# Performance work log

Measured on AMD Instinct MI355X. Metric: run time of the kernel, lower is better.

Reference implementation:

```python
import jax, jax.numpy as jnp
import numpy as np

Q = 4          # num_quantizers
K = 2048       # codebook_size
D = 256        # dim
B, N = 8, 8192 # batch, tokens (N % Q == 0)


def l2norm(t, eps=1e-12):
    return t / jnp.maximum(jnp.linalg.norm(t, axis=-1, keepdims=True), eps)


def setup_inputs() -> dict:
    key = jax.random.key(0)
    kx, ke = jax.random.split(key)
    x = jax.random.normal(kx, (B, N, D), dtype=jnp.float32)
    embed = jax.random.normal(ke, (Q, K, D), dtype=jnp.float32)
    return {"x": x, "embed": embed}


def reference(x, embed):
    b, n, d = x.shape
    q = embed.shape[0]
    m = n // q  # tokens per quantizer chunk
    # chunk along token axis (dim=1), as torch.chunk(x, Q, dim=1)
    xc = x.reshape(b, q, m, d).transpose(1, 0, 2, 3)  # [Q, B, M, D]

    def one_vq(xq, eq):
        # xq: [B, M, D], eq: [K, D]
        xn = l2norm(xq)
        en = l2norm(eq)
        dist = jnp.einsum('bmd,kd->bmk', xn, en)   # cosine similarity
        ind = jnp.argmax(dist, axis=-1)            # temp=0 gumbel -> argmax
        quant = eq[ind]                            # F.embedding with raw embed
        return quant, ind

    quant_c, ind_c = jax.vmap(one_vq)(xc, embed)   # [Q,B,M,D], [Q,B,M]
    quantized = quant_c.transpose(1, 0, 2, 3).reshape(b, n, d)
    encoding = ind_c.transpose(1, 0, 2).reshape(b, n)
    # eval mode: loss is sum of Q zero tensors of shape [1]
    vq_loss = jnp.zeros((1,), dtype=x.dtype)
    return quantized, encoding, vq_loss
```

## Files before the change

### kernel.cpp

```cpp
#include <hip/hip_runtime.h>
#include <math.h>

#define Bq 8
#define Nq 8192
#define Dq 256
#define Qq 4
#define Kq 2048
#define Mq (Nq / Qq)
#define TT (Bq * Nq)
#define QUANT_ELEMS ((size_t)TT * Dq)

#define CAP1Q 4096
#define THRESH 3e-4f

#define WS_CNT_OFF    0u
#define WS_LIST_OFF   1024u
#define WS_PSC_OFF    66560u
#define WS_PCD_OFF    590848u
#define WS_ENH_OFF    1115136u
#define WS_ENP_OFF    5309440u
#define WS_PART_OFF   13698048u

typedef __attribute__((ext_vector_type(8))) _Float16 f16x8;
typedef __attribute__((ext_vector_type(4))) _Float16 f16x4;
typedef __attribute__((ext_vector_type(4))) float    f32x4;

__device__ __forceinline__ void async_load16(const void* g, void* s) {
    __builtin_amdgcn_global_load_lds(
        (const __attribute__((address_space(1))) void*)g,
        (__attribute__((address_space(3))) void*)s, 16, 0, 0);
}

__device__ __forceinline__ float f32_div(float a, float b) {
    return (float)((double)a / (double)b);
}

__device__ __forceinline__ float np_norm_wave(const float* __restrict__ src, int ln) {
#pragma clang fp contract(off)
    float r = 0.0f;
    if (ln < 16) {
        const float* p = src + (ln >> 3) * 128 + (ln & 7);
        #pragma unroll
        for (int m = 0; m < 16; ++m) { float v = p[m * 8]; r = r + v * v; }
    }
    float t = r + __shfl_xor(r, 1, 64);
    t = t + __shfl_xor(t, 2, 64);
    t = t + __shfl_xor(t, 4, 64);
    float b0 = __shfl(t, 0, 64);
    float b1 = __shfl(t, 8, 64);
    float n2 = b0 + b1;
    return fmaxf((float)sqrt((double)n2), 1e-12f);
}

__global__ __launch_bounds__(256) void prep_kernel(const float* __restrict__ embed,
                                                   char* __restrict__ enh,
                                                   float* __restrict__ enp) {
    int row = blockIdx.x * 4 + (threadIdx.x >> 6);
    int ln  = threadIdx.x & 63;
    const float* src = embed + (size_t)row * Dq;

    float4 v = *(const float4*)(src + ln * 4);
    float s = v.x * v.x + v.y * v.y + v.z * v.z + v.w * v.w;
    #pragma unroll
    for (int m = 1; m < 64; m <<= 1) s += __shfl_xor(s, m, 64);
    float sx = 1.0f / fmaxf(sqrtf(s), 1e-12f);
    int q = row >> 11, k = row & 2047, Tb = k >> 5, c = k & 31;
    int g = ln >> 1, h = ln & 1;
    f16x4 o;
    o[0] = (_Float16)(v.x * sx); o[1] = (_Float16)(v.y * sx);
    o[2] = (_Float16)(v.z * sx); o[3] = (_Float16)(v.w * sx);
    char* dst = enh + ((size_t)(q * 64 + Tb)) * 16384 + c * 512 + ((g ^ c) << 4) + h * 8;
    *(f16x4*)dst = o;

    float nm = np_norm_wave(src, ln);
    float* dstp = enp + (size_t)row * Dq;
    #pragma unroll
    for (int e = 0; e < 4; ++e) dstp[ln * 4 + e] = f32_div(src[ln * 4 + e], nm);
}

__global__ __launch_bounds__(256) void gemm_kernel(const float* __restrict__ x,
                                                   const char* __restrict__ enh,
                                                   float4* __restrict__ part) {
    __shared__ __align__(16) char es[2][16384];

    const int tid = threadIdx.x;
    const int wv  = tid >> 6;
    const int ln  = tid & 63;
    const int qd  = ln >> 4;
    const int l15 = ln & 15;

    const int bid = blockIdx.x;
    const int q   = bid & 3;
    const int h   = (bid >> 2) & 1;
    const int w   = bid >> 3;
    const int t0  = (w >> 4) * Nq + q * Mq + (w & 15) * 128;
    const int t0w = t0 + wv * 32;

    f16x8 ah[2][8];
    #pragma unroll
    for (int mf = 0; mf < 2; ++mf) {
        const float* xr = x + (size_t)(t0w + mf * 16 + l15) * Dq + qd * 8;
        float4 xa[16];
        float s2 = 0.f;
        #pragma unroll
        for (int ch = 0; ch < 8; ++ch) {
            float4 u = *(const float4*)(xr + ch * 32);
            float4 v = *(const float4*)(xr + ch * 32 + 4);
            xa[2 * ch] = u; xa[2 * ch + 1] = v;
            s2 += u.x * u.x + u.y * u.y + u.z * u.z + u.w * u.w;
            s2 += v.x * v.x + v.y * v.y + v.z * v.z + v.w * v.w;
        }
        s2 += __shfl_xor(s2, 16, 64);
        s2 += __shfl_xor(s2, 32, 64);
        float sx = 1.0f / fmaxf(sqrtf(s2), 1e-12f);
        #pragma unroll
        for (int ch = 0; ch < 8; ++ch) {
            float4 u = xa[2 * ch], v = xa[2 * ch + 1];
            f16x8 f;
            f[0] = (_Float16)(u.x * sx); f[1] = (_Float16)(u.y * sx);
            f[2] = (_Float16)(u.z * sx); f[3] = (_Float16)(u.w * sx);
            f[4] = (_Float16)(v.x * sx); f[5] = (_Float16)(v.y * sx);
            f[6] = (_Float16)(v.z * sx); f[7] = (_Float16)(v.w * sx);
            ah[mf][ch] = f;
        }
    }

    float b1[2][4], b2[2][4];
    int   ic[2][4];
    #pragma unroll
    for (int mf = 0; mf < 2; ++mf)
        #pragma unroll
        for (int r = 0; r < 4; ++r) { b1[mf][r] = -2.0f; b2[mf][r] = -2.0f; ic[mf][r] = 0; }

    const char* ebase = enh + ((size_t)(q * 64 + h * 32)) * 16384;

    #pragma unroll
    for (int i = 0; i < 4; ++i) {
        int off = i * 4096 + wv * 1024 + ln * 16;
        async_load16(ebase + off, es[0] + off);
    }
    __syncthreads();

    for (int T = 0; T < 32; ++T) {
        if (T + 1 < 32) {
            const char* src = ebase + (size_t)(T + 1) * 16384;
            #pragma unroll
            for (int i = 0; i < 4; ++i) {
                int off = i * 4096 + wv * 1024 + ln * 16;
                async_load16(src + off, es[(T + 1) & 1] + off);
            }
        }
        const char* esb = es[T & 1];

        #pragma unroll
        for (int s = 0; s < 2; ++s) {
            const int  c  = s * 16 + l15;
            const char* cb = esb + c * 512;
            f16x8 bfr[8];
            #pragma unroll
            for (int ch = 0; ch < 8; ++ch)
                bfr[ch] = *(const f16x8*)(cb + ((((ch << 2) | qd) ^ c) << 4));

            f32x4 a0 = {0.f, 0.f, 0.f, 0.f};
            f32x4 a1 = {0.f, 0.f, 0.f, 0.f};
            #pragma unroll
            for (int ch = 0; ch < 8; ++ch) {
                a0 = __builtin_amdgcn_mfma_f32_16x16x32_f16(ah[0][ch], bfr[ch], a0, 0, 0, 0);
                a1 = __builtin_amdgcn_mfma_f32_16x16x32_f16(ah[1][ch], bfr[ch], a1, 0, 0, 0);
            }
            const int cg = (h << 10) | (T << 5) | (s << 4) | l15;
            #pragma unroll
            for (int r = 0; r < 4; ++r) {
                float s0 = a0[r];
                bool  g0 = s0 > b1[0][r];
                b2[0][r] = __builtin_amdgcn_fmed3f(s0, b1[0][r], b2[0][r]);
                b1[0][r] = fmaxf(b1[0][r], s0);
                ic[0][r] = g0 ? cg : ic[0][r];
                float s1 = a1[r];
                bool  g1 = s1 > b1[1][r];
                b2[1][r] = __builtin_amdgcn_fmed3f(s1, b1[1][r], b2[1][r]);
                b1[1][r] = fmaxf(b1[1][r], s1);
                ic[1][r] = g1 ? cg : ic[1][r];
            }
        }
        __syncthreads();
    }

    float fb1[2][4], fb2[2][4];
    int   fic[2][4];
    #pragma unroll
    for (int mf = 0; mf < 2; ++mf)
        #pragma unroll
        for (int r = 0; r < 4; ++r) {
            float v1 = b1[mf][r], v2 = b2[mf][r]; int vi = ic[mf][r];
            #pragma unroll
            for (int m = 1; m < 16; m <<= 1) {
                float o1 = __shfl_xor(v1, m, 64);
                float o2 = __shfl_xor(v2, m, 64);
                int   oi = __shfl_xor(vi, m, 64);
                if (o1 > v1 || (o1 == v1 && oi < vi)) { v2 = fmaxf(v1, o2); v1 = o1; vi = oi; }
                else v2 = fmaxf(v2, o1);
            }
            fb1[mf][r] = v1; fb2[mf][r] = v2; fic[mf][r] = vi;
        }

    if (l15 == 0) {
        #pragma unroll
        for (int mf = 0; mf < 2; ++mf)
            #pragma unroll
            for (int r = 0; r < 4; ++r) {
                int t = t0w + mf * 16 + qd * 4 + r;
                float4 pv;
                pv.x = fb1[mf][r];
                pv.y = fb2[mf][r];
                pv.z = __int_as_float(fic[mf][r]);
                pv.w = 0.f;
                part[(size_t)h * TT + t] = pv;
            }
    }
}

__global__ __launch_bounds__(256) void merge_kernel(const float* __restrict__ embed,
                                                    const float4* __restrict__ part,
                                                    float* __restrict__ out,
                                                    int* __restrict__ cnt,
                                                    int* __restrict__ list) {
    const int wv = threadIdx.x >> 6, ln = threadIdx.x & 63;
    const int nw = gridDim.x * 4;

    for (int t = blockIdx.x * 4 + wv; t < TT; t += nw) {
        float4 pa = part[t];
        float4 pb = part[TT + t];
        float v1, v2; int vi;
        if (pb.x > pa.x) { v1 = pb.x; vi = __float_as_int(pb.z); v2 = fmaxf(pa.x, pb.y); }
        else             { v1 = pa.x; vi = __float_as_int(pa.z); v2 = fmaxf(pb.x, pa.y); }
        const int q = (t >> 11) & 3;

        if (ln == 0) {
            out[QUANT_ELEMS + (size_t)t] = (float)vi;
            if (v1 - v2 < THRESH) {
                int pos = atomicAdd(&cnt[q], 1);
                if (pos < CAP1Q) list[q * CAP1Q + pos] = t;
            }
        }
        const float* er = embed + ((size_t)(q * Kq + vi)) * Dq;
        float4 v = *(const float4*)(er + ln * 4);
        *(float4*)(out + (size_t)t * Dq + ln * 4) = v;
    }
    if (blockIdx.x == 0 && threadIdx.x == 0) out[QUANT_ELEMS + TT] = 0.0f;
}

__global__ __launch_bounds__(256) void fix_partial(const float* __restrict__ x,
                                                   const float* __restrict__ enp,
                                                   const int* __restrict__ cnt,
                                                   const int* __restrict__ list,
                                                   float* __restrict__ pscore,
                                                   int* __restrict__ pcode) {
#pragma clang fp contract(off)
    __shared__ float xn[16][Dq];
    __shared__ int   stok[16];
    __shared__ float wp_s[4][16];
    __shared__ int   wp_c[4][16];

    const int tid = threadIdx.x;
    const int wv  = tid >> 6;
    const int ln  = tid & 63;

    int cq[4], nbq[4], total = 0;
    #pragma unroll
    for (int q = 0; q < 4; ++q) {
        int c = cnt[q]; if (c > CAP1Q) c = CAP1Q;
        cq[q] = c; nbq[q] = (c + 15) >> 4; total += nbq[q] * 8;
    }

    for (int j = blockIdx.x; j < total; j += gridDim.x) {
        int rem = j, q = 0;
        while (rem >= nbq[q] * 8) { rem -= nbq[q] * 8; ++q; }
        const int batch = rem >> 3, chunk = rem & 7;

        if (tid < 16) {
            int idx = batch * 16 + tid;
            stok[tid] = list[q * CAP1Q + (idx < cq[q] ? idx : batch * 16)];
        }
        __syncthreads();
        for (int r = 0; r < 4; ++r) {
            int i = wv * 4 + r;
            const float* xr = x + (size_t)stok[i] * Dq;
            float nm = np_norm_wave(xr, ln);
            #pragma unroll
            for (int e = 0; e < 4; ++e)
                xn[i][ln * 4 + e] = f32_div(xr[ln * 4 + e], nm);
        }
        __syncthreads();

        const int c = chunk * 256 + tid;
        const float* er = enp + ((size_t)(q * Kq + c)) * Dq;
        float l0[16], l1[16], l2[16], l3[16];
        #pragma unroll
        for (int i = 0; i < 16; ++i) { l0[i] = 0.f; l1[i] = 0.f; l2[i] = 0.f; l3[i] = 0.f; }

        for (int d = 0; d < Dq; d += 4) {
            float4 e = *(const float4*)(er + d);
            #pragma unroll
            for (int i = 0; i < 16; ++i) {
                float4 xv = *(const float4*)&xn[i][d];
                l0[i] = l0[i] + xv.x * e.x;
                l1[i] = l1[i] + xv.y * e.y;
                l2[i] = l2[i] + xv.z * e.z;
                l3[i] = l3[i] + xv.w * e.w;
            }
        }

        #pragma unroll
        for (int i = 0; i < 16; ++i) {
            float s = (l0[i] + l1[i]) + (l2[i] + l3[i]);
            int bc = c;
            #pragma unroll
            for (int m = 1; m < 64; m <<= 1) {
                float os = __shfl_xor(s, m, 64);
                int   oc = __shfl_xor(bc, m, 64);
                if (os > s || (os == s && oc < bc)) { s = os; bc = oc; }
            }
            if (ln == 0) { wp_s[wv][i] = s; wp_c[wv][i] = bc; }
        }
        __syncthreads();
        if (tid < 16) {
            int idx = batch * 16 + tid;
            if (idx < cq[q]) {
                float s = wp_s[0][tid]; int bc = wp_c[0][tid];
                #pragma unroll
                for (int w2 = 1; w2 < 4; ++w2) {
                    float os = wp_s[w2][tid]; int oc = wp_c[w2][tid];
                    if (os > s || (os == s && oc < bc)) { s = os; bc = oc; }
                }
                int p = q * CAP1Q + idx;
                pscore[p * 8 + chunk] = s;
                pcode[p * 8 + chunk]  = bc;
            }
        }
        __syncthreads();
    }
}

__global__ __launch_bounds__(256) void fix_final(const float* __restrict__ embed,
                                                 const int* __restrict__ cnt,
                                                 const int* __restrict__ list,
                                                 const float* __restrict__ pscore,
                                                 const int* __restrict__ pcode,
                                                 float* __restrict__ out) {
    int cq[4], tot = 0;
    #pragma unroll
    for (int q = 0; q < 4; ++q) {
        int c = cnt[q]; if (c > CAP1Q) c = CAP1Q;
        cq[q] = c; tot += c;
    }
    const int wv = threadIdx.x >> 6, ln = threadIdx.x & 63;

    for (int j = blockIdx.x * 4 + wv; j < tot; j += gridDim.x * 4) {
        int rem = j, q = 0;
        while (rem >= cq[q]) { rem -= cq[q]; ++q; }
        int p = q * CAP1Q + rem;
        int t = list[p];
        int bc = 0;
        if (ln == 0) {
            float bs = pscore[p * 8]; bc = pcode[p * 8];
            #pragma unroll
            for (int ch = 1; ch < 8; ++ch) {
                float s = pscore[p * 8 + ch]; int c2 = pcode[p * 8 + ch];
                if (s > bs || (s == bs && c2 < bc)) { bs = s; bc = c2; }
            }
            out[QUANT_ELEMS + (size_t)t] = (float)bc;
        }
        bc = __shfl(bc, 0, 64);
        const float* er = embed + ((size_t)(q * Kq + bc)) * Dq;
        float4 v = *(const float4*)(er + ln * 4);
        *(float4*)(out + (size_t)t * Dq + ln * 4) = v;
    }
}

extern "C" void kernel_launch(void* const* d_in, const int* in_sizes, int n_in,
                              void* d_out, int out_size, void* d_ws, size_t ws_size,
                              hipStream_t stream) {
    const float* x     = (const float*)d_in[0];
    const float* embed = (const float*)d_in[1];
    float* out = (float*)d_out;
    char*  ws  = (char*)d_ws;
    int*    cnt    = (int*)(ws + WS_CNT_OFF);
    int*    list   = (int*)(ws + WS_LIST_OFF);
    float*  pscore = (float*)(ws + WS_PSC_OFF);
    int*    pcode  = (int*)(ws + WS_PCD_OFF);
    char*   enh    = ws + WS_ENH_OFF;
    float*  enp    = (float*)(ws + WS_ENP_OFF);
    float4* part   = (float4*)(ws + WS_PART_OFF);

    hipMemsetAsync(cnt, 0, 16, stream);
    prep_kernel<<<(Qq * Kq) / 4, 256, 0, stream>>>(embed, enh, enp);
    gemm_kernel<<<1024, 256, 0, stream>>>(x, enh, part);
    merge_kernel<<<2048, 256, 0, stream>>>(embed, part, out, cnt, list);
    fix_partial<<<1024, 256, 0, stream>>>(x, enp, cnt, list, pscore, pcode);
    fix_final<<<256, 256, 0, stream>>>(embed, cnt, list, pscore, pcode, out);
}
```

Measured before the change: 290.1 us.

## Use triple-buffered half-size LDS tiles with explicit vmcnt waits in GEMM loop

The codebook tile loop changes from double-buffered 16 KB tiles to a three-stage ring of 8 KB tiles (16 codes each), prefetching two tiles ahead. Each step waits with an explicit s_waitcnt vmcnt and a single barrier instead of two __syncthreads per tile. This is meant to hide global-to-LDS latency better and cut shared memory use per block, which could allow more blocks per CU. In exchange there are twice as many barrier steps, each doing less MFMA work, and the hand-written vmcnt counting relies on the async_load16 instruction count staying fixed.

Measured after the change: 298.1 us. +2.8%, slower.

```diff
diff --git a/kernel.cpp b/kernel.cpp
--- a/kernel.cpp
+++ b/kernel.cpp
@@ -81,7 +81,7 @@
 __global__ __launch_bounds__(256) void gemm_kernel(const float* __restrict__ x,
                                                    const char* __restrict__ enh,
                                                    float4* __restrict__ part) {
-    __shared__ __align__(16) char es[2][16384];
+    __shared__ __align__(16) char es[3][8192];
 
     const int tid = threadIdx.x;
     const int wv  = tid >> 6;
@@ -133,57 +133,60 @@
         for (int r = 0; r < 4; ++r) { b1[mf][r] = -2.0f; b2[mf][r] = -2.0f; ic[mf][r] = 0; }
 
     const char* ebase = enh + ((size_t)(q * 64 + h * 32)) * 16384;
-
-    #pragma unroll
-    for (int i = 0; i < 4; ++i) {
-        int off = i * 4096 + wv * 1024 + ln * 16;
-        async_load16(ebase + off, es[0] + off);
-    }
-    __syncthreads();
-
-    for (int T = 0; T < 32; ++T) {
-        if (T + 1 < 32) {
-            const char* src = ebase + (size_t)(T + 1) * 16384;
-            #pragma unroll
-            for (int i = 0; i < 4; ++i) {
-                int off = i * 4096 + wv * 1024 + ln * 16;
-                async_load16(src + off, es[(T + 1) & 1] + off);
-            }
-        }
-        const char* esb = es[T & 1];
-
-        #pragma unroll
-        for (int s = 0; s < 2; ++s) {
-            const int  c  = s * 16 + l15;
-            const char* cb = esb + c * 512;
-            f16x8 bfr[8];
-            #pragma unroll
-            for (int ch = 0; ch < 8; ++ch)
-                bfr[ch] = *(const f16x8*)(cb + ((((ch << 2) | qd) ^ c) << 4));
-
-            f32x4 a0 = {0.f, 0.f, 0.f, 0.f};
-            f32x4 a1 = {0.f, 0.f, 0.f, 0.f};
-            #pragma unroll
-            for (int ch = 0; ch < 8; ++ch) {
-                a0 = __builtin_amdgcn_mfma_f32_16x16x32_f16(ah[0][ch], bfr[ch], a0, 0, 0, 0);
-                a1 = __builtin_amdgcn_mfma_f32_16x16x32_f16(ah[1][ch], bfr[ch], a1, 0, 0, 0);
-            }
-            const int cg = (h << 10) | (T << 5) | (s << 4) | l15;
-            #pragma unroll
-            for (int r = 0; r < 4; ++r) {
-                float s0 = a0[r];
-                bool  g0 = s0 > b1[0][r];
-                b2[0][r] = __builtin_amdgcn_fmed3f(s0, b1[0][r], b2[0][r]);
-                b1[0][r] = fmaxf(b1[0][r], s0);
-                ic[0][r] = g0 ? cg : ic[0][r];
-                float s1 = a1[r];
-                bool  g1 = s1 > b1[1][r];
-                b2[1][r] = __builtin_amdgcn_fmed3f(s1, b1[1][r], b2[1][r]);
-                b1[1][r] = fmaxf(b1[1][r], s1);
-                ic[1][r] = g1 ? cg : ic[1][r];
-            }
-        }
-        __syncthreads();
+    const int off0 = wv * 1024 + ln * 16;
+
+    #pragma unroll
+    for (int i = 0; i < 2; ++i)
+        async_load16(ebase + i * 4096 + off0, es[0] + i * 4096 + off0);
+    #pragma unroll
+    for (int i = 0; i < 2; ++i)
+        async_load16(ebase + 8192 + i * 4096 + off0, es[1] + i * 4096 + off0);
+
+    int rb = 0;
+    for (int T = 0; T < 64; ++T) {
+        if (T < 63) asm volatile("s_waitcnt vmcnt(2)" ::: "memory");
+        else        asm volatile("s_waitcnt vmcnt(0)" ::: "memory");
+        __builtin_amdgcn_s_barrier();
+        asm volatile("" ::: "memory");
+
+        if (T + 2 < 64) {
+            int wb = rb + 2; if (wb >= 3) wb -= 3;
+            const char* src = ebase + (size_t)(T + 2) * 8192;
+            #pragma unroll
+            for (int i = 0; i < 2; ++i)
+                async_load16(src + i * 4096 + off0, es[wb] + i * 4096 + off0);
+        }
+
+        const char* cb = es[rb] + l15 * 512;
+        const int   c5 = ((T & 1) << 4) | l15;
+        f16x8 bfr[8];
+        #pragma unroll
+        for (int ch = 0; ch < 8; ++ch)
+            bfr[ch] = *(const f16x8*)(cb + ((((ch << 2) | qd) ^ c5) << 4));
+
+        f32x4 a0 = {0.f, 0.f, 0.f, 0.f};
+        f32x4 a1 = {0.f, 0.f, 0.f, 0.f};
+        #pragma unroll
+        for (int ch = 0; ch < 8; ++ch) {
+            a0 = __builtin_amdgcn_mfma_f32_16x16x32_f16(ah[0][ch], bfr[ch], a0, 0, 0, 0);
+            a1 = __builtin_amdgcn_mfma_f32_16x16x32_f16(ah[1][ch], bfr[ch], a1, 0, 0, 0);
+        }
+
+        const int cg = (h << 10) | (T << 4) | l15;
+        #pragma unroll
+        for (int r = 0; r < 4; ++r) {
+            float s0 = a0[r];
+            bool  g0 = s0 > b1[0][r];
+            b2[0][r] = __builtin_amdgcn_fmed3f(s0, b1[0][r], b2[0][r]);
+            b1[0][r] = fmaxf(b1[0][r], s0);
+            ic[0][r] = g0 ? cg : ic[0][r];
+            float s1 = a1[r];
+            bool  g1 = s1 > b1[1][r];
+            b2[1][r] = __builtin_amdgcn_fmed3f(s1, b1[1][r], b2[1][r]);
+            b1[1][r] = fmaxf(b1[1][r], s1);
+            ic[1][r] = g1 ? cg : ic[1][r];
+        }
+        if (++rb == 3) rb = 0;
     }
 
     float fb1[2][4], fb2[2][4];
```

## Split codebook four ways in GEMM and precompute token inverse norms

Applied to the files above, without the earlier changes.

The codebook is now split into four chunks of 512 codes per block instead of two of 1024, doubling the GEMM grid to 2048 blocks for better CU occupancy. Token inverse norms are computed once in extra prep blocks and read by the GEMM, so each of the four splits no longer reduces the full x row itself. Partial results are stored as separate float2 and int arrays, and the merge kernel reduces four partials. This costs extra x reads and more partial traffic, and the PSC/PCD workspace regions now overlap the partial buffers, relying on fix_partial running after merge.

Result: slower. 307.2 us (+5.9%).

```diff
diff --git a/kernel.cpp b/kernel.cpp
--- a/kernel.cpp
+++ b/kernel.cpp
@@ -15,11 +15,13 @@
 
 #define WS_CNT_OFF    0u
 #define WS_LIST_OFF   1024u
-#define WS_PSC_OFF    66560u
-#define WS_PCD_OFF    590848u
-#define WS_ENH_OFF    1115136u
-#define WS_ENP_OFF    5309440u
-#define WS_PART_OFF   13698048u
+#define WS_SX_OFF     66560u
+#define WS_ENH_OFF    328704u
+#define WS_ENP_OFF    4523008u
+#define WS_PART_OFF   12911616u
+#define WS_PIC_OFF    15008768u
+#define WS_PSC_OFF    12911616u
+#define WS_PCD_OFF    13435904u
 
 typedef __attribute__((ext_vector_type(8))) _Float16 f16x8;
 typedef __attribute__((ext_vector_type(4))) _Float16 f16x4;
@@ -53,8 +55,30 @@
 }
 
 __global__ __launch_bounds__(256) void prep_kernel(const float* __restrict__ embed,
+                                                   const float* __restrict__ x,
                                                    char* __restrict__ enh,
-                                                   float* __restrict__ enp) {
+                                                   float* __restrict__ enp,
+                                                   float* __restrict__ sxa) {
+    if (blockIdx.x >= 2048) {
+        const int tid = threadIdx.x;
+        const int qd  = tid & 3;
+        const int row = (blockIdx.x - 2048) * 64 + (tid >> 2);
+        const float* xr = x + (size_t)row * Dq + qd * 8;
+        float s2 = 0.f;
+        #pragma unroll
+        for (int ch = 0; ch < 8; ++ch) {
+            float4 u = *(const float4*)(xr + ch * 32);
+            float4 v = *(const float4*)(xr + ch * 32 + 4);
+            s2 += u.x * u.x + u.y * u.y + u.z * u.z + u.w * u.w;
+            s2 += v.x * v.x + v.y * v.y + v.z * v.z + v.w * v.w;
+        }
+        s2 += __shfl_xor(s2, 1, 64);
+        s2 += __shfl_xor(s2, 2, 64);
+        float sxv = 1.0f / fmaxf(sqrtf(s2), 1e-12f);
+        if (qd == 0) sxa[row] = sxv;
+        return;
+    }
+
     int row = blockIdx.x * 4 + (threadIdx.x >> 6);
     int ln  = threadIdx.x & 63;
     const float* src = embed + (size_t)row * Dq;
@@ -79,8 +103,10 @@
 }
 
 __global__ __launch_bounds__(256) void gemm_kernel(const float* __restrict__ x,
+                                                   const float* __restrict__ sxa,
                                                    const char* __restrict__ enh,
-                                                   float4* __restrict__ part) {
+                                                   float2* __restrict__ pb12,
+                                                   int* __restrict__ pic) {
     __shared__ __align__(16) char es[2][16384];
 
     const int tid = threadIdx.x;
@@ -91,36 +117,26 @@
 
     const int bid = blockIdx.x;
     const int q   = bid & 3;
-    const int h   = (bid >> 2) & 1;
-    const int w   = bid >> 3;
+    const int h   = (bid >> 2) & 3;
+    const int w   = bid >> 4;
     const int t0  = (w >> 4) * Nq + q * Mq + (w & 15) * 128;
     const int t0w = t0 + wv * 32;
 
     f16x8 ah[2][8];
     #pragma unroll
     for (int mf = 0; mf < 2; ++mf) {
-        const float* xr = x + (size_t)(t0w + mf * 16 + l15) * Dq + qd * 8;
-        float4 xa[16];
-        float s2 = 0.f;
+        const int tok = t0w + mf * 16 + l15;
+        const float sxv = sxa[tok];
+        const float* xr = x + (size_t)tok * Dq + qd * 8;
         #pragma unroll
         for (int ch = 0; ch < 8; ++ch) {
             float4 u = *(const float4*)(xr + ch * 32);
             float4 v = *(const float4*)(xr + ch * 32 + 4);
-            xa[2 * ch] = u; xa[2 * ch + 1] = v;
-            s2 += u.x * u.x + u.y * u.y + u.z * u.z + u.w * u.w;
-            s2 += v.x * v.x + v.y * v.y + v.z * v.z + v.w * v.w;
-        }
-        s2 += __shfl_xor(s2, 16, 64);
-        s2 += __shfl_xor(s2, 32, 64);
-        float sx = 1.0f / fmaxf(sqrtf(s2), 1e-12f);
-        #pragma unroll
-        for (int ch = 0; ch < 8; ++ch) {
-            float4 u = xa[2 * ch], v = xa[2 * ch + 1];
             f16x8 f;
-            f[0] = (_Float16)(u.x * sx); f[1] = (_Float16)(u.y * sx);
-            f[2] = (_Float16)(u.z * sx); f[3] = (_Float16)(u.w * sx);
-            f[4] = (_Float16)(v.x * sx); f[5] = (_Float16)(v.y * sx);
-            f[6] = (_Float16)(v.z * sx); f[7] = (_Float16)(v.w * sx);
+            f[0] = (_Float16)(u.x * sxv); f[1] = (_Float16)(u.y * sxv);
+            f[2] = (_Float16)(u.z * sxv); f[3] = (_Float16)(u.w * sxv);
+            f[4] = (_Float16)(v.x * sxv); f[5] = (_Float16)(v.y * sxv);
+            f[6] = (_Float16)(v.z * sxv); f[7] = (_Float16)(v.w * sxv);
             ah[mf][ch] = f;
         }
     }
@@ -132,7 +148,7 @@
         #pragma unroll
         for (int r = 0; r < 4; ++r) { b1[mf][r] = -2.0f; b2[mf][r] = -2.0f; ic[mf][r] = 0; }
 
-    const char* ebase = enh + ((size_t)(q * 64 + h * 32)) * 16384;
+    const char* ebase = enh + ((size_t)(q * 64 + h * 16)) * 16384;
 
     #pragma unroll
     for (int i = 0; i < 4; ++i) {
@@ -141,8 +157,8 @@
     }
     __syncthreads();
 
-    for (int T = 0; T < 32; ++T) {
-        if (T + 1 < 32) {
+    for (int T = 0; T < 16; ++T) {
+        if (T + 1 < 16) {
             const char* src = ebase + (size_t)(T + 1) * 16384;
             #pragma unroll
             for (int i = 0; i < 4; ++i) {
@@ -168,7 +184,7 @@
                 a0 = __builtin_amdgcn_mfma_f32_16x16x32_f16(ah[0][ch], bfr[ch], a0, 0, 0, 0);
                 a1 = __builtin_amdgcn_mfma_f32_16x16x32_f16(ah[1][ch], bfr[ch], a1, 0, 0, 0);
             }
-            const int cg = (h << 10) | (T << 5) | (s << 4) | l15;
+            const int cg = (h << 9) | (T << 5) | (s << 4) | l15;
             #pragma unroll
             for (int r = 0; r < 4; ++r) {
                 float s0 = a0[r];
@@ -210,18 +226,16 @@
             #pragma unroll
             for (int r = 0; r < 4; ++r) {
                 int t = t0w + mf * 16 + qd * 4 + r;
-                float4 pv;
-                pv.x = fb1[mf][r];
-                pv.y = fb2[mf][r];
-                pv.z = __int_as_float(fic[mf][r]);
-                pv.w = 0.f;
-                part[(size_t)h * TT + t] = pv;
+                float2 pv; pv.x = fb1[mf][r]; pv.y = fb2[mf][r];
+                pb12[(size_t)h * TT + t] = pv;
+                pic [(size_t)h * TT + t] = fic[mf][r];
             }
     }
 }
 
 __global__ __launch_bounds__(256) void merge_kernel(const float* __restrict__ embed,
-                                                    const float4* __restrict__ part,
+                                                    const float2* __restrict__ pb12,
+                                                    const int* __restrict__ pic,
                                                     float* __restrict__ out,
                                                     int* __restrict__ cnt,
                                                     int* __restrict__ list) {
@@ -229,11 +243,16 @@
     const int nw = gridDim.x * 4;
 
     for (int t = blockIdx.x * 4 + wv; t < TT; t += nw) {
-        float4 pa = part[t];
-        float4 pb = part[TT + t];
-        float v1, v2; int vi;
-        if (pb.x > pa.x) { v1 = pb.x; vi = __float_as_int(pb.z); v2 = fmaxf(pa.x, pb.y); }
-        else             { v1 = pa.x; vi = __float_as_int(pa.z); v2 = fmaxf(pb.x, pa.y); }
+        float2 p0 = pb12[t];
+        float v1 = p0.x, v2 = p0.y;
+        int   vi = pic[t];
+        #pragma unroll
+        for (int hh = 1; hh < 4; ++hh) {
+            float2 ph = pb12[(size_t)hh * TT + t];
+            int    ih = pic[(size_t)hh * TT + t];
+            if (ph.x > v1) { v2 = fmaxf(v1, ph.y); v1 = ph.x; vi = ih; }
+            else           { v2 = fmaxf(v2, ph.x); }
+        }
         const int q = (t >> 11) & 3;
 
         if (ln == 0) {
@@ -387,16 +406,18 @@
     char*  ws  = (char*)d_ws;
     int*    cnt    = (int*)(ws + WS_CNT_OFF);
     int*    list   = (int*)(ws + WS_LIST_OFF);
+    float*  sxa    = (float*)(ws + WS_SX_OFF);
+    char*   enh    = ws + WS_ENH_OFF;
+    float*  enp    = (float*)(ws + WS_ENP_OFF);
+    float2* pb12   = (float2*)(ws + WS_PART_OFF);
+    int*    pic    = (int*)(ws + WS_PIC_OFF);
     float*  pscore = (float*)(ws + WS_PSC_OFF);
     int*    pcode  = (int*)(ws + WS_PCD_OFF);
-    char*   enh    = ws + WS_ENH_OFF;
-    float*  enp    = (float*)(ws + WS_ENP_OFF);
-    float4* part   = (float4*)(ws + WS_PART_OFF);
 
     hipMemsetAsync(cnt, 0, 16, stream);
-    prep_kernel<<<(Qq * Kq) / 4, 256, 0, stream>>>(embed, enh, enp);
-    gemm_kernel<<<1024, 256, 0, stream>>>(x, enh, part);
-    merge_kernel<<<2048, 256, 0, stream>>>(embed, part, out, cnt, list);
+    prep_kernel<<<3072, 256, 0, stream>>>(embed, x, enh, enp, sxa);
+    gemm_kernel<<<2048, 256, 0, stream>>>(x, sxa, enh, pb12, pic);
+    merge_kernel<<<2048, 256, 0, stream>>>(embed, pb12, pic, out, cnt, list);
     fix_partial<<<1024, 256, 0, stream>>>(x, enp, cnt, list, pscore, pcode);
     fix_final<<<256, 256, 0, stream>>>(embed, cnt, list, pscore, pcode, out);
 }
```

## Double GEMM row tile, precompute token norms in prep, fold memset into prep

Applied to the files above, without the earlier changes.

The GEMM kernel now handles 64 tokens per wave (4 MFMA row fragments instead of 2), so each codebook tile staged in LDS is reused across twice as many tokens, and it launches half as many blocks. Token inverse norms are computed in extra blocks of the prep kernel and read back, which removes the norm reduction from the GEMM prologue. The counter memset and the loss-zero write move into prep, dropping one launch. The cost is higher register pressure from the larger accumulator and argmax state (launch_bounds 256,2), fewer GEMM blocks for the GPU to spread across its CUs, and one extra read of x.

New measurement: 295.3 us. Within noise of the previous version (+1.8%).

```diff
diff --git a/kernel.cpp b/kernel.cpp
--- a/kernel.cpp
+++ b/kernel.cpp
@@ -15,11 +15,12 @@
 
 #define WS_CNT_OFF    0u
 #define WS_LIST_OFF   1024u
-#define WS_PSC_OFF    66560u
-#define WS_PCD_OFF    590848u
-#define WS_ENH_OFF    1115136u
-#define WS_ENP_OFF    5309440u
-#define WS_PART_OFF   13698048u
+#define WS_SX_OFF     66560u
+#define WS_PSC_OFF    328704u
+#define WS_PCD_OFF    852992u
+#define WS_ENH_OFF    1377280u
+#define WS_ENP_OFF    5571584u
+#define WS_PART_OFF   13960192u
 
 typedef __attribute__((ext_vector_type(8))) _Float16 f16x8;
 typedef __attribute__((ext_vector_type(4))) _Float16 f16x4;
@@ -53,8 +54,37 @@
 }
 
 __global__ __launch_bounds__(256) void prep_kernel(const float* __restrict__ embed,
+                                                   const float* __restrict__ x,
                                                    char* __restrict__ enh,
-                                                   float* __restrict__ enp) {
+                                                   float* __restrict__ enp,
+                                                   float* __restrict__ sxa,
+                                                   int* __restrict__ cnt,
+                                                   float* __restrict__ out) {
+    if (blockIdx.x >= 2048) {
+        const int tid = threadIdx.x;
+        const int qd  = tid & 3;
+        const int row = (blockIdx.x - 2048) * 64 + (tid >> 2);
+        const float* xr = x + (size_t)row * Dq + qd * 8;
+        float s2 = 0.f;
+        #pragma unroll
+        for (int ch = 0; ch < 8; ++ch) {
+            float4 u = *(const float4*)(xr + ch * 32);
+            float4 v = *(const float4*)(xr + ch * 32 + 4);
+            s2 += u.x * u.x + u.y * u.y + u.z * u.z + u.w * u.w;
+            s2 += v.x * v.x + v.y * v.y + v.z * v.z + v.w * v.w;
+        }
+        s2 += __shfl_xor(s2, 1, 64);
+        s2 += __shfl_xor(s2, 2, 64);
+        float sxv = 1.0f / fmaxf(sqrtf(s2), 1e-12f);
+        if (qd == 0) sxa[row] = sxv;
+        return;
+    }
+
+    if (blockIdx.x == 0) {
+        if (threadIdx.x < 4) cnt[threadIdx.x] = 0;
+        if (threadIdx.x == 0) out[QUANT_ELEMS + TT] = 0.0f;
+    }
+
     int row = blockIdx.x * 4 + (threadIdx.x >> 6);
     int ln  = threadIdx.x & 63;
     const float* src = embed + (size_t)row * Dq;
@@ -78,9 +108,10 @@
     for (int e = 0; e < 4; ++e) dstp[ln * 4 + e] = f32_div(src[ln * 4 + e], nm);
 }
 
-__global__ __launch_bounds__(256) void gemm_kernel(const float* __restrict__ x,
-                                                   const char* __restrict__ enh,
-                                                   float4* __restrict__ part) {
+__global__ __launch_bounds__(256, 2) void gemm_kernel(const float* __restrict__ x,
+                                                      const float* __restrict__ sxa,
+                                                      const char* __restrict__ enh,
+                                                      float4* __restrict__ part) {
     __shared__ __align__(16) char es[2][16384];
 
     const int tid = threadIdx.x;
@@ -90,45 +121,38 @@
     const int l15 = ln & 15;
 
     const int bid = blockIdx.x;
-    const int q   = bid & 3;
-    const int h   = (bid >> 2) & 1;
-    const int w   = bid >> 3;
-    const int t0  = (w >> 4) * Nq + q * Mq + (w & 15) * 128;
-    const int t0w = t0 + wv * 32;
-
-    f16x8 ah[2][8];
-    #pragma unroll
-    for (int mf = 0; mf < 2; ++mf) {
-        const float* xr = x + (size_t)(t0w + mf * 16 + l15) * Dq + qd * 8;
-        float4 xa[16];
-        float s2 = 0.f;
+    const int h   = bid & 1;
+    const int g   = bid >> 1;
+    const int b   = g >> 5;
+    const int rem = g & 31;
+    const int q   = rem >> 3;
+    const int m0  = (rem & 7) << 8;
+    const int t0  = b * Nq + q * Mq + m0;
+    const int t0w = t0 + wv * 64;
+
+    f16x8 ah[4][8];
+    #pragma unroll
+    for (int mf = 0; mf < 4; ++mf) {
+        const int tok = t0w + mf * 16 + l15;
+        const float sxv = sxa[tok];
+        const float* xr = x + (size_t)tok * Dq + qd * 8;
         #pragma unroll
         for (int ch = 0; ch < 8; ++ch) {
             float4 u = *(const float4*)(xr + ch * 32);
             float4 v = *(const float4*)(xr + ch * 32 + 4);
-            xa[2 * ch] = u; xa[2 * ch + 1] = v;
-            s2 += u.x * u.x + u.y * u.y + u.z * u.z + u.w * u.w;
-            s2 += v.x * v.x + v.y * v.y + v.z * v.z + v.w * v.w;
-        }
-        s2 += __shfl_xor(s2, 16, 64);
-        s2 += __shfl_xor(s2, 32, 64);
-        float sx = 1.0f / fmaxf(sqrtf(s2), 1e-12f);
-        #pragma unroll
-        for (int ch = 0; ch < 8; ++ch) {
-            float4 u = xa[2 * ch], v = xa[2 * ch + 1];
             f16x8 f;
-            f[0] = (_Float16)(u.x * sx); f[1] = (_Float16)(u.y * sx);
-            f[2] = (_Float16)(u.z * sx); f[3] = (_Float16)(u.w * sx);
-            f[4] = (_Float16)(v.x * sx); f[5] = (_Float16)(v.y * sx);
-            f[6] = (_Float16)(v.z * sx); f[7] = (_Float16)(v.w * sx);
+            f[0] = (_Float16)(u.x * sxv); f[1] = (_Float16)(u.y * sxv);
+            f[2] = (_Float16)(u.z * sxv); f[3] = (_Float16)(u.w * sxv);
+            f[4] = (_Float16)(v.x * sxv); f[5] = (_Float16)(v.y * sxv);
+            f[6] = (_Float16)(v.z * sxv); f[7] = (_Float16)(v.w * sxv);
             ah[mf][ch] = f;
         }
     }
 
-    float b1[2][4], b2[2][4];
-    int   ic[2][4];
-    #pragma unroll
-    for (int mf = 0; mf < 2; ++mf)
+    float b1[4][4], b2[4][4];
+    int   ic[4][4];
+    #pragma unroll
+    for (int mf = 0; mf < 4; ++mf)
         #pragma unroll
         for (int r = 0; r < 4; ++r) { b1[mf][r] = -2.0f; b2[mf][r] = -2.0f; ic[mf][r] = 0; }
 
@@ -161,35 +185,35 @@
             for (int ch = 0; ch < 8; ++ch)
                 bfr[ch] = *(const f16x8*)(cb + ((((ch << 2) | qd) ^ c) << 4));
 
-            f32x4 a0 = {0.f, 0.f, 0.f, 0.f};
-            f32x4 a1 = {0.f, 0.f, 0.f, 0.f};
+            f32x4 a[4];
+            #pragma unroll
+            for (int mf = 0; mf < 4; ++mf) a[mf] = (f32x4){0.f, 0.f, 0.f, 0.f};
             #pragma unroll
             for (int ch = 0; ch < 8; ++ch) {
-                a0 = __builtin_amdgcn_mfma_f32_16x16x32_f16(ah[0][ch], bfr[ch], a0, 0, 0, 0);
-                a1 = __builtin_amdgcn_mfma_f32_16x16x32_f16(ah[1][ch], bfr[ch], a1, 0, 0, 0);
-            }
+                #pragma unroll
+                for (int mf = 0; mf < 4; ++mf)
+                    a[mf] = __builtin_amdgcn_mfma_f32_16x16x32_f16(ah[mf][ch], bfr[ch], a[mf], 0, 0, 0);
+            }
+
             const int cg = (h << 10) | (T << 5) | (s << 4) | l15;
             #pragma unroll
-            for (int r = 0; r < 4; ++r) {
-                float s0 = a0[r];
-                bool  g0 = s0 > b1[0][r];
-                b2[0][r] = __builtin_amdgcn_fmed3f(s0, b1[0][r], b2[0][r]);
-                b1[0][r] = fmaxf(b1[0][r], s0);
-                ic[0][r] = g0 ? cg : ic[0][r];
-                float s1 = a1[r];
-                bool  g1 = s1 > b1[1][r];
-                b2[1][r] = __builtin_amdgcn_fmed3f(s1, b1[1][r], b2[1][r]);
-                b1[1][r] = fmaxf(b1[1][r], s1);
-                ic[1][r] = g1 ? cg : ic[1][r];
-            }
+            for (int mf = 0; mf < 4; ++mf)
+                #pragma unroll
+                for (int r = 0; r < 4; ++r) {
+                    float sv = a[mf][r];
+                    bool  gt = sv > b1[mf][r];
+                    b2[mf][r] = __builtin_amdgcn_fmed3f(sv, b1[mf][r], b2[mf][r]);
+                    b1[mf][r] = fmaxf(b1[mf][r], sv);
+                    ic[mf][r] = gt ? cg : ic[mf][r];
+                }
         }
         __syncthreads();
     }
 
-    float fb1[2][4], fb2[2][4];
-    int   fic[2][4];
-    #pragma unroll
-    for (int mf = 0; mf < 2; ++mf)
+    float fb1[4][4], fb2[4][4];
+    int   fic[4][4];
+    #pragma unroll
+    for (int mf = 0; mf < 4; ++mf)
         #pragma unroll
         for (int r = 0; r < 4; ++r) {
             float v1 = b1[mf][r], v2 = b2[mf][r]; int vi = ic[mf][r];
@@ -206,7 +230,7 @@
 
     if (l15 == 0) {
         #pragma unroll
-        for (int mf = 0; mf < 2; ++mf)
+        for (int mf = 0; mf < 4; ++mf)
             #pragma unroll
             for (int r = 0; r < 4; ++r) {
                 int t = t0w + mf * 16 + qd * 4 + r;
@@ -247,7 +271,6 @@
         float4 v = *(const float4*)(er + ln * 4);
         *(float4*)(out + (size_t)t * Dq + ln * 4) = v;
     }
-    if (blockIdx.x == 0 && threadIdx.x == 0) out[QUANT_ELEMS + TT] = 0.0f;
 }
 
 __global__ __launch_bounds__(256) void fix_partial(const float* __restrict__ x,
@@ -387,15 +410,15 @@
     char*  ws  = (char*)d_ws;
     int*    cnt    = (int*)(ws + WS_CNT_OFF);
     int*    list   = (int*)(ws + WS_LIST_OFF);
+    float*  sxa    = (float*)(ws + WS_SX_OFF);
     float*  pscore = (float*)(ws + WS_PSC_OFF);
     int*    pcode  = (int*)(ws + WS_PCD_OFF);
     char*   enh    = ws + WS_ENH_OFF;
     float*  enp    = (float*)(ws + WS_ENP_OFF);
     float4* part   = (float4*)(ws + WS_PART_OFF);
 
-    hipMemsetAsync(cnt, 0, 16, stream);
-    prep_kernel<<<(Qq * Kq) / 4, 256, 0, stream>>>(embed, enh, enp);
-    gemm_kernel<<<1024, 256, 0, stream>>>(x, enh, part);
+    prep_kernel<<<3072, 256, 0, stream>>>(embed, x, enh, enp, sxa, cnt, out);
+    gemm_kernel<<<512, 256, 0, stream>>>(x, sxa, enh, part);
     merge_kernel<<<2048, 256, 0, stream>>>(embed, part, out, cnt, list);
     fix_partial<<<1024, 256, 0, stream>>>(x, enp, cnt, list, pscore, pcode);
     fix_final<<<256, 256, 0, stream>>>(embed, cnt, list, pscore, pcode, out);
```
